# Kernel optimization log

Measured on AMD Instinct MI355X. Metric: run time of the kernel, lower is better.

The kernel has to match this reference:

```python
import jax, jax.numpy as jnp
import numpy as np

C, S, H = 64, 2048, 512
ITERATIONS = 3

def squash(x, eps=1e-07):
    # per-vector squash along last dim: (|x|^2/(1+|x|^2)) * x/|x|
    sq = jnp.sum(x * x, axis=-1, keepdims=True)
    safe_norm = jnp.sqrt(sq + eps)
    scale = sq / (1.0 + sq)
    return scale * (x / safe_norm)

def setup_inputs() -> dict:
    key = jax.random.key(0)
    k1, k2 = jax.random.split(key)
    x = jax.random.normal(k1, (C * S, H), dtype=jnp.float32)
    # xavier-normal init for Linear(H, H)
    std = np.sqrt(2.0 / (H + H)).astype(np.float32)
    W_weight = jax.random.normal(k2, (H, H), dtype=jnp.float32) * std
    W_bias = jnp.zeros((H,), dtype=jnp.float32)
    return {"x": x, "W_weight": W_weight, "W_bias": W_bias}

def reference(x, W_weight, W_bias):
    xr = x.reshape(C, S, H)
    # e_ij = squash(Linear(x))  -> [C, S, H]
    e_ij = squash(jnp.einsum('csh,oh->cso', xr, W_weight) + W_bias)
    b_ij = jnp.zeros((C, S), dtype=x.dtype)
    c_i = jnp.zeros((C, H), dtype=x.dtype)
    for _ in range(ITERATIONS):
        d_i = jax.nn.softmax(b_ij, axis=1)[..., None]          # [C, S, 1]
        c_i = squash(jnp.sum(d_i * e_ij, axis=1))              # [C, H]
        b_ij = b_ij + jnp.einsum('csh,ch->cs', e_ij, c_i)      # [C, S]
    return c_i
```

## Files before the change

kernel.cpp:

```cpp
#include <hip/hip_runtime.h>
#include <hip/hip_bf16.h>
#include <hip/hip_fp16.h>

#define HDIM 512
#define NROWS 131072
#define NCAPS 64

typedef __attribute__((ext_vector_type(8))) short short8;
typedef __attribute__((ext_vector_type(4))) float floatx4;

__device__ __forceinline__ unsigned short f2bf(float f) {
  unsigned u = __float_as_uint(f);
  u += 0x7FFFu + ((u >> 16) & 1u);
  return (unsigned short)(u >> 16);
}
__device__ __forceinline__ float bf2f(unsigned short h) {
  return __uint_as_float(((unsigned)h) << 16);
}

__global__ __launch_bounds__(256) void prep_w_kernel(
    const float* __restrict__ W, unsigned short* __restrict__ wh,
    unsigned short* __restrict__ wl) {
  int i = (blockIdx.x * 256 + threadIdx.x) * 4;
  float4 f = *(const float4*)(W + i);
  float fv[4] = {f.x, f.y, f.z, f.w};
#pragma unroll
  for (int j = 0; j < 4; ++j) {
    unsigned short h = f2bf(fv[j]);
    wh[i + j] = h;
    wl[i + j] = f2bf(fv[j] - bf2f(h));
  }
}

#define BM 128
#define BN 128
#define BK 64

__global__ __launch_bounds__(256) void gemm_kernel(
    const float* __restrict__ x, const unsigned short* __restrict__ wh,
    const unsigned short* __restrict__ wl, const float* __restrict__ bias,
    __half* __restrict__ y, float* __restrict__ sq) {
  __shared__ unsigned short xs[BM * BK];
  __shared__ unsigned short whs[BN * BK];
  __shared__ unsigned short wls[BN * BK];

  const int tid = threadIdx.x;
  const int lane = tid & 63;
  const int widx = tid >> 6;
  const int wave_m = widx >> 1, wave_n = widx & 1;
  const int lrow = lane & 15, quad = lane >> 4, l7 = lane & 7;

  const int bid = blockIdx.x;
  const int m_blk = ((bid >> 5) << 3) + (bid & 7);
  const int n_blk = (bid >> 3) & 3;
  const int row0 = m_blk * BM;
  const int col0 = n_blk * BN;

  floatx4 acc[4][4];
#pragma unroll
  for (int i = 0; i < 4; ++i)
#pragma unroll
    for (int j = 0; j < 4; ++j) acc[i][j] = (floatx4){0.f, 0.f, 0.f, 0.f};

  const int xm = tid >> 3;
  const int xkg = tid & 7;
  const int wn_sub = lane >> 3;
  const int wphys = lane & 7;

  for (int kt = 0; kt < 8; ++kt) {
    const int k0 = kt * BK;
    __syncthreads();
#pragma unroll
    for (int p = 0; p < 4; ++p) {
      int m = p * 32 + xm;
      const float* gp = x + (size_t)(row0 + m) * HDIM + k0 + xkg * 8;
      float4 f0 = *(const float4*)gp;
      float4 f1 = *(const float4*)(gp + 4);
      short8 v;
      v[0] = (short)f2bf(f0.x); v[1] = (short)f2bf(f0.y);
      v[2] = (short)f2bf(f0.z); v[3] = (short)f2bf(f0.w);
      v[4] = (short)f2bf(f1.x); v[5] = (short)f2bf(f1.y);
      v[6] = (short)f2bf(f1.z); v[7] = (short)f2bf(f1.w);
      int phys = xkg ^ (m & 7);
      *(short8*)&xs[m * 64 + phys * 8] = v;
    }
#pragma unroll
    for (int q = 0; q < 4; ++q) {
      int i = widx * 4 + q;
      int n_loc = 8 * i + wn_sub;
      int kg_l = wphys ^ (n_loc & 7);
      size_t goff = (size_t)(col0 + n_loc) * HDIM + k0 + kg_l * 8;
      __builtin_amdgcn_global_load_lds(
          (const __attribute__((address_space(1))) void*)(wh + goff),
          (__attribute__((address_space(3))) void*)&whs[i * 512], 16, 0, 0);
      __builtin_amdgcn_global_load_lds(
          (const __attribute__((address_space(1))) void*)(wl + goff),
          (__attribute__((address_space(3))) void*)&wls[i * 512], 16, 0, 0);
    }
    __syncthreads();
#pragma unroll
    for (int ks = 0; ks < 2; ++ks) {
      int physA = (ks * 4 + quad) ^ l7;
      short8 a[4], bh[4], bl[4];
#pragma unroll
      for (int mt = 0; mt < 4; ++mt) {
        int r = wave_m * 64 + mt * 16 + lrow;
        a[mt] = *(const short8*)&xs[r * 64 + physA * 8];
      }
#pragma unroll
      for (int nt = 0; nt < 4; ++nt) {
        int c = wave_n * 64 + nt * 16 + lrow;
        bh[nt] = *(const short8*)&whs[c * 64 + physA * 8];
        bl[nt] = *(const short8*)&wls[c * 64 + physA * 8];
      }
#pragma unroll
      for (int mt = 0; mt < 4; ++mt)
#pragma unroll
        for (int nt = 0; nt < 4; ++nt) {
          acc[mt][nt] = __builtin_amdgcn_mfma_f32_16x16x32_bf16(
              a[mt], bh[nt], acc[mt][nt], 0, 0, 0);
          acc[mt][nt] = __builtin_amdgcn_mfma_f32_16x16x32_bf16(
              a[mt], bl[nt], acc[mt][nt], 0, 0, 0);
        }
    }
  }

  int colg[4];
  float bias_v[4];
#pragma unroll
  for (int nt = 0; nt < 4; ++nt) {
    colg[nt] = col0 + wave_n * 64 + nt * 16 + lrow;
    bias_v[nt] = bias[colg[nt]];
  }
#pragma unroll
  for (int mt = 0; mt < 4; ++mt) {
#pragma unroll
    for (int r = 0; r < 4; ++r) {
      int rowg = row0 + wave_m * 64 + mt * 16 + quad * 4 + r;
      float s = 0.f;
#pragma unroll
      for (int nt = 0; nt < 4; ++nt) {
        float yv = acc[mt][nt][r] + bias_v[nt];
        s += yv * yv;
        y[(size_t)rowg * HDIM + colg[nt]] = __float2half(yv);
      }
      s += __shfl_xor(s, 1, 64);
      s += __shfl_xor(s, 2, 64);
      s += __shfl_xor(s, 4, 64);
      s += __shfl_xor(s, 8, 64);
      if (lrow == 0) atomicAdd(&sq[rowg], s);
    }
  }
}

__global__ __launch_bounds__(256) void scale_kernel(const float* __restrict__ sq,
                                                    float* __restrict__ scale) {
  int i = blockIdx.x * 256 + threadIdx.x;
  float s = sq[i];
  scale[i] = s / ((1.f + s) * sqrtf(s + 1e-7f));
}

__global__ __launch_bounds__(256) void kbv_kernel(
    const __half* __restrict__ y, const float* __restrict__ scale,
    float* __restrict__ b, const float* __restrict__ c_buf,
    float* __restrict__ u_part, float* __restrict__ den_part) {
  const int wave_g = blockIdx.x * 4 + (threadIdx.x >> 6);
  const int lane = threadIdx.x & 63;
  const int cap = wave_g >> 6;
  const int chunk = wave_g & 63;
  const int r0 = cap * 2048 + chunk * 32;

  float c8[8];
  {
    const float4* cp = (const float4*)(c_buf + cap * HDIM + lane * 8);
    float4 ca = cp[0], cb = cp[1];
    c8[0] = ca.x; c8[1] = ca.y; c8[2] = ca.z; c8[3] = ca.w;
    c8[4] = cb.x; c8[5] = cb.y; c8[6] = cb.z; c8[7] = cb.w;
  }
  float u8[8] = {0, 0, 0, 0, 0, 0, 0, 0};
  float den = 0.f;

  union U { int4 v; __half h[8]; };
  U cur;
  cur.v = *(const int4*)(y + (size_t)r0 * HDIM + lane * 8);

  for (int i = 0; i < 32; ++i) {
    int r = r0 + i;
    U nxt;
    if (i < 31) nxt.v = *(const int4*)(y + (size_t)(r + 1) * HDIM + lane * 8);
    float f[8];
#pragma unroll
    for (int j = 0; j < 8; ++j) f[j] = __half2float(cur.h[j]);
    float dot = f[0] * c8[0] + f[1] * c8[1] + f[2] * c8[2] + f[3] * c8[3] +
                f[4] * c8[4] + f[5] * c8[5] + f[6] * c8[6] + f[7] * c8[7];
    dot += __shfl_xor(dot, 1, 64);
    dot += __shfl_xor(dot, 2, 64);
    dot += __shfl_xor(dot, 4, 64);
    dot += __shfl_xor(dot, 8, 64);
    dot += __shfl_xor(dot, 16, 64);
    dot += __shfl_xor(dot, 32, 64);
    float sc = scale[r];
    float bn = b[r] + sc * dot;
    if (lane == 0) b[r] = bn;
    float w = expf(bn);
    den += w;
    float wsc = w * sc;
#pragma unroll
    for (int j = 0; j < 8; ++j) u8[j] += wsc * f[j];
    cur = nxt;
  }
  float* up = u_part + (size_t)(cap * 64 + chunk) * HDIM + lane * 8;
  *(float4*)up = (float4){u8[0], u8[1], u8[2], u8[3]};
  *(float4*)(up + 4) = (float4){u8[4], u8[5], u8[6], u8[7]};
  if (lane == 0) den_part[cap * 64 + chunk] = den;
}

__global__ __launch_bounds__(256) void kcsq_kernel(
    const float* __restrict__ u_part, const float* __restrict__ den_part,
    float* __restrict__ out) {
  const int cap = blockIdx.x;
  const int t = threadIdx.x;
  __shared__ float red[256];
  __shared__ float sden;

  float d = 0.f;
  if (t < 64) d = den_part[cap * 64 + t];
  red[t] = d;
  __syncthreads();
  if (t == 0) {
    float s = 0.f;
    for (int i = 0; i < 64; ++i) s += red[i];
    sden = s;
  }
  __syncthreads();
  const float den = sden;

  float v0 = 0.f, v1 = 0.f;
  for (int ch = 0; ch < 64; ++ch) {
    const float* up = u_part + (size_t)(cap * 64 + ch) * HDIM;
    v0 += up[t];
    v1 += up[t + 256];
  }
  v0 /= den;
  v1 /= den;

  red[t] = v0 * v0 + v1 * v1;
  __syncthreads();
  for (int s = 128; s > 0; s >>= 1) {
    if (t < s) red[t] += red[t + s];
    __syncthreads();
  }
  const float sqv = red[0];
  const float scv = sqv / ((1.f + sqv) * sqrtf(sqv + 1e-7f));
  out[cap * HDIM + t] = v0 * scv;
  out[cap * HDIM + t + 256] = v1 * scv;
}

extern "C" void kernel_launch(void* const* d_in, const int* in_sizes, int n_in,
                              void* d_out, int out_size, void* d_ws,
                              size_t ws_size, hipStream_t stream) {
  const float* x = (const float*)d_in[0];
  const float* W = (const float*)d_in[1];
  const float* bias = (const float*)d_in[2];
  float* out = (float*)d_out;
  char* ws = (char*)d_ws;

  __half* y = (__half*)ws;
  float* sq = (float*)(ws + (size_t)134217728);
  float* b = sq + 131072;
  float* c_buf = b + 131072;
  float* scale = c_buf + 32768;
  unsigned short* wh = (unsigned short*)(scale + 131072);
  unsigned short* wl = wh + 262144;
  float* u_part = (float*)(wl + 262144);
  float* den_part = u_part + (size_t)64 * 64 * 512;

  hipMemsetAsync(sq, 0, (size_t)(131072 + 131072 + 32768) * sizeof(float),
                 stream);

  prep_w_kernel<<<256, 256, 0, stream>>>(W, wh, wl);
  gemm_kernel<<<4096, 256, 0, stream>>>(x, wh, wl, bias, y, sq);
  scale_kernel<<<512, 256, 0, stream>>>(sq, scale);

  for (int it = 0; it < 3; ++it) {
    kbv_kernel<<<1024, 256, 0, stream>>>(y, scale, b, c_buf, u_part, den_part);
    kcsq_kernel<<<64, 256, 0, stream>>>(u_part, den_part,
                                        (it == 2) ? out : c_buf);
  }
}
```

Before: 586.7 us.

## Switch GEMM to single fp16 MFMA, fuse scale into routing, batch rows

The GEMM now converts x and W to fp16 and runs one f16 MFMA per tile pair, replacing the two-pass bf16 hi/lo split of W. This halves the MFMA work and the weight LDS traffic, at the cost of fp16 range and precision on the inputs (round-toward-zero packing). The separate scale kernel is removed and the squash scale is recomputed inside the routing kernel. That kernel now processes four rows at a time with interleaved shuffles and uses fast exp. The reduce kernel uses 512 threads with one column each.

```diff
diff --git a/kernel.cpp b/kernel.cpp
--- a/kernel.cpp
+++ b/kernel.cpp
@@ -1,35 +1,20 @@
 #include <hip/hip_runtime.h>
-#include <hip/hip_bf16.h>
 #include <hip/hip_fp16.h>
 
 #define HDIM 512
-#define NROWS 131072
-#define NCAPS 64
-
-typedef __attribute__((ext_vector_type(8))) short short8;
+
+typedef __fp16 fp16x2 __attribute__((ext_vector_type(2)));
+typedef _Float16 h8 __attribute__((ext_vector_type(8)));
 typedef __attribute__((ext_vector_type(4))) float floatx4;
 
-__device__ __forceinline__ unsigned short f2bf(float f) {
-  unsigned u = __float_as_uint(f);
-  u += 0x7FFFu + ((u >> 16) & 1u);
-  return (unsigned short)(u >> 16);
-}
-__device__ __forceinline__ float bf2f(unsigned short h) {
-  return __uint_as_float(((unsigned)h) << 16);
-}
-
 __global__ __launch_bounds__(256) void prep_w_kernel(
-    const float* __restrict__ W, unsigned short* __restrict__ wh,
-    unsigned short* __restrict__ wl) {
+    const float* __restrict__ W, _Float16* __restrict__ wf) {
   int i = (blockIdx.x * 256 + threadIdx.x) * 4;
   float4 f = *(const float4*)(W + i);
-  float fv[4] = {f.x, f.y, f.z, f.w};
-#pragma unroll
-  for (int j = 0; j < 4; ++j) {
-    unsigned short h = f2bf(fv[j]);
-    wh[i + j] = h;
-    wl[i + j] = f2bf(fv[j] - bf2f(h));
-  }
+  wf[i + 0] = (_Float16)f.x;
+  wf[i + 1] = (_Float16)f.y;
+  wf[i + 2] = (_Float16)f.z;
+  wf[i + 3] = (_Float16)f.w;
 }
 
 #define BM 128
@@ -37,12 +22,11 @@
 #define BK 64
 
 __global__ __launch_bounds__(256) void gemm_kernel(
-    const float* __restrict__ x, const unsigned short* __restrict__ wh,
-    const unsigned short* __restrict__ wl, const float* __restrict__ bias,
-    __half* __restrict__ y, float* __restrict__ sq) {
-  __shared__ unsigned short xs[BM * BK];
-  __shared__ unsigned short whs[BN * BK];
-  __shared__ unsigned short wls[BN * BK];
+    const float* __restrict__ x, const _Float16* __restrict__ wf,
+    const float* __restrict__ bias, __half* __restrict__ y,
+    float* __restrict__ sq) {
+  __shared__ _Float16 xs[BM * BK];
+  __shared__ _Float16 wsm[BN * BK];
 
   const int tid = threadIdx.x;
   const int lane = tid & 63;
@@ -76,13 +60,13 @@
       const float* gp = x + (size_t)(row0 + m) * HDIM + k0 + xkg * 8;
       float4 f0 = *(const float4*)gp;
       float4 f1 = *(const float4*)(gp + 4);
-      short8 v;
-      v[0] = (short)f2bf(f0.x); v[1] = (short)f2bf(f0.y);
-      v[2] = (short)f2bf(f0.z); v[3] = (short)f2bf(f0.w);
-      v[4] = (short)f2bf(f1.x); v[5] = (short)f2bf(f1.y);
-      v[6] = (short)f2bf(f1.z); v[7] = (short)f2bf(f1.w);
+      union { h8 v8; fp16x2 v2[4]; } u;
+      u.v2[0] = __builtin_amdgcn_cvt_pkrtz(f0.x, f0.y);
+      u.v2[1] = __builtin_amdgcn_cvt_pkrtz(f0.z, f0.w);
+      u.v2[2] = __builtin_amdgcn_cvt_pkrtz(f1.x, f1.y);
+      u.v2[3] = __builtin_amdgcn_cvt_pkrtz(f1.z, f1.w);
       int phys = xkg ^ (m & 7);
-      *(short8*)&xs[m * 64 + phys * 8] = v;
+      *(h8*)&xs[m * 64 + phys * 8] = u.v8;
     }
 #pragma unroll
     for (int q = 0; q < 4; ++q) {
@@ -91,37 +75,30 @@
       int kg_l = wphys ^ (n_loc & 7);
       size_t goff = (size_t)(col0 + n_loc) * HDIM + k0 + kg_l * 8;
       __builtin_amdgcn_global_load_lds(
-          (const __attribute__((address_space(1))) void*)(wh + goff),
-          (__attribute__((address_space(3))) void*)&whs[i * 512], 16, 0, 0);
-      __builtin_amdgcn_global_load_lds(
-          (const __attribute__((address_space(1))) void*)(wl + goff),
-          (__attribute__((address_space(3))) void*)&wls[i * 512], 16, 0, 0);
+          (const __attribute__((address_space(1))) void*)(wf + goff),
+          (__attribute__((address_space(3))) void*)&wsm[i * 512], 16, 0, 0);
     }
     __syncthreads();
 #pragma unroll
     for (int ks = 0; ks < 2; ++ks) {
       int physA = (ks * 4 + quad) ^ l7;
-      short8 a[4], bh[4], bl[4];
+      h8 a[4], bh[4];
 #pragma unroll
       for (int mt = 0; mt < 4; ++mt) {
         int r = wave_m * 64 + mt * 16 + lrow;
-        a[mt] = *(const short8*)&xs[r * 64 + physA * 8];
+        a[mt] = *(const h8*)&xs[r * 64 + physA * 8];
       }
 #pragma unroll
       for (int nt = 0; nt < 4; ++nt) {
         int c = wave_n * 64 + nt * 16 + lrow;
-        bh[nt] = *(const short8*)&whs[c * 64 + physA * 8];
-        bl[nt] = *(const short8*)&wls[c * 64 + physA * 8];
+        bh[nt] = *(const h8*)&wsm[c * 64 + physA * 8];
       }
 #pragma unroll
       for (int mt = 0; mt < 4; ++mt)
 #pragma unroll
-        for (int nt = 0; nt < 4; ++nt) {
-          acc[mt][nt] = __builtin_amdgcn_mfma_f32_16x16x32_bf16(
+        for (int nt = 0; nt < 4; ++nt)
+          acc[mt][nt] = __builtin_amdgcn_mfma_f32_16x16x32_f16(
               a[mt], bh[nt], acc[mt][nt], 0, 0, 0);
-          acc[mt][nt] = __builtin_amdgcn_mfma_f32_16x16x32_bf16(
-              a[mt], bl[nt], acc[mt][nt], 0, 0, 0);
-        }
     }
   }
 
@@ -153,15 +130,8 @@
   }
 }
 
-__global__ __launch_bounds__(256) void scale_kernel(const float* __restrict__ sq,
-                                                    float* __restrict__ scale) {
-  int i = blockIdx.x * 256 + threadIdx.x;
-  float s = sq[i];
-  scale[i] = s / ((1.f + s) * sqrtf(s + 1e-7f));
-}
-
 __global__ __launch_bounds__(256) void kbv_kernel(
-    const __half* __restrict__ y, const float* __restrict__ scale,
+    const __half* __restrict__ y, const float* __restrict__ sqbuf,
     float* __restrict__ b, const float* __restrict__ c_buf,
     float* __restrict__ u_part, float* __restrict__ den_part) {
   const int wave_g = blockIdx.x * 4 + (threadIdx.x >> 6);
@@ -180,34 +150,51 @@
   float u8[8] = {0, 0, 0, 0, 0, 0, 0, 0};
   float den = 0.f;
 
-  union U { int4 v; __half h[8]; };
-  U cur;
-  cur.v = *(const int4*)(y + (size_t)r0 * HDIM + lane * 8);
-
-  for (int i = 0; i < 32; ++i) {
-    int r = r0 + i;
-    U nxt;
-    if (i < 31) nxt.v = *(const int4*)(y + (size_t)(r + 1) * HDIM + lane * 8);
-    float f[8];
-#pragma unroll
-    for (int j = 0; j < 8; ++j) f[j] = __half2float(cur.h[j]);
-    float dot = f[0] * c8[0] + f[1] * c8[1] + f[2] * c8[2] + f[3] * c8[3] +
-                f[4] * c8[4] + f[5] * c8[5] + f[6] * c8[6] + f[7] * c8[7];
-    dot += __shfl_xor(dot, 1, 64);
-    dot += __shfl_xor(dot, 2, 64);
-    dot += __shfl_xor(dot, 4, 64);
-    dot += __shfl_xor(dot, 8, 64);
-    dot += __shfl_xor(dot, 16, 64);
-    dot += __shfl_xor(dot, 32, 64);
-    float sc = scale[r];
-    float bn = b[r] + sc * dot;
-    if (lane == 0) b[r] = bn;
-    float w = expf(bn);
-    den += w;
-    float wsc = w * sc;
-#pragma unroll
-    for (int j = 0; j < 8; ++j) u8[j] += wsc * f[j];
-    cur = nxt;
+  union U { int4 v; __half hh[8]; };
+  U cur[4], nxt[4];
+  const __half* yb = y + (size_t)r0 * HDIM + lane * 8;
+#pragma unroll
+  for (int j = 0; j < 4; ++j) cur[j].v = *(const int4*)(yb + (size_t)j * HDIM);
+
+  for (int g = 0; g < 8; ++g) {
+    const int rg = r0 + g * 4;
+    if (g < 7) {
+#pragma unroll
+      for (int j = 0; j < 4; ++j)
+        nxt[j].v = *(const int4*)(yb + (size_t)(g * 4 + 4 + j) * HDIM);
+    }
+    float sc[4], bv[4];
+#pragma unroll
+    for (int j = 0; j < 4; ++j) {
+      float s = sqbuf[rg + j];
+      sc[j] = s / ((1.f + s) * sqrtf(s + 1e-7f));
+      bv[j] = b[rg + j];
+    }
+    float dot[4];
+#pragma unroll
+    for (int j = 0; j < 4; ++j) {
+      float d = 0.f;
+#pragma unroll
+      for (int k = 0; k < 8; ++k) d += __half2float(cur[j].hh[k]) * c8[k];
+      dot[j] = d;
+    }
+#pragma unroll
+    for (int s = 1; s < 64; s <<= 1) {
+#pragma unroll
+      for (int j = 0; j < 4; ++j) dot[j] += __shfl_xor(dot[j], s, 64);
+    }
+#pragma unroll
+    for (int j = 0; j < 4; ++j) {
+      float bn = bv[j] + sc[j] * dot[j];
+      if (lane == 0) b[rg + j] = bn;
+      float w = __expf(bn);
+      den += w;
+      float wsc = w * sc[j];
+#pragma unroll
+      for (int k = 0; k < 8; ++k) u8[k] += wsc * __half2float(cur[j].hh[k]);
+    }
+#pragma unroll
+    for (int j = 0; j < 4; ++j) cur[j] = nxt[j];
   }
   float* up = u_part + (size_t)(cap * 64 + chunk) * HDIM + lane * 8;
   *(float4*)up = (float4){u8[0], u8[1], u8[2], u8[3]};
@@ -215,45 +202,37 @@
   if (lane == 0) den_part[cap * 64 + chunk] = den;
 }
 
-__global__ __launch_bounds__(256) void kcsq_kernel(
+__global__ __launch_bounds__(512) void kcsq_kernel(
     const float* __restrict__ u_part, const float* __restrict__ den_part,
     float* __restrict__ out) {
   const int cap = blockIdx.x;
   const int t = threadIdx.x;
-  __shared__ float red[256];
-  __shared__ float sden;
-
-  float d = 0.f;
-  if (t < 64) d = den_part[cap * 64 + t];
+  __shared__ float red[512];
+
+  float d = (t < 64) ? den_part[cap * 64 + t] : 0.f;
   red[t] = d;
   __syncthreads();
-  if (t == 0) {
-    float s = 0.f;
-    for (int i = 0; i < 64; ++i) s += red[i];
-    sden = s;
-  }
+  for (int s = 256; s > 0; s >>= 1) {
+    if (t < s) red[t] += red[t + s];
+    __syncthreads();
+  }
+  const float den = red[0];
   __syncthreads();
-  const float den = sden;
-
-  float v0 = 0.f, v1 = 0.f;
-  for (int ch = 0; ch < 64; ++ch) {
-    const float* up = u_part + (size_t)(cap * 64 + ch) * HDIM;
-    v0 += up[t];
-    v1 += up[t + 256];
-  }
-  v0 /= den;
-  v1 /= den;
-
-  red[t] = v0 * v0 + v1 * v1;
+
+  float v = 0.f;
+  const float* up = u_part + (size_t)cap * 64 * HDIM + t;
+  for (int ch = 0; ch < 64; ++ch) v += up[ch * HDIM];
+  v /= den;
+
+  red[t] = v * v;
   __syncthreads();
-  for (int s = 128; s > 0; s >>= 1) {
+  for (int s = 256; s > 0; s >>= 1) {
     if (t < s) red[t] += red[t + s];
     __syncthreads();
   }
   const float sqv = red[0];
   const float scv = sqv / ((1.f + sqv) * sqrtf(sqv + 1e-7f));
-  out[cap * HDIM + t] = v0 * scv;
-  out[cap * HDIM + t + 256] = v1 * scv;
+  out[cap * HDIM + t] = v * scv;
 }
 
 extern "C" void kernel_launch(void* const* d_in, const int* in_sizes, int n_in,
@@ -269,22 +248,20 @@
   float* sq = (float*)(ws + (size_t)134217728);
   float* b = sq + 131072;
   float* c_buf = b + 131072;
-  float* scale = c_buf + 32768;
-  unsigned short* wh = (unsigned short*)(scale + 131072);
-  unsigned short* wl = wh + 262144;
-  float* u_part = (float*)(wl + 262144);
+  _Float16* wf = (_Float16*)(c_buf + 32768);
+  float* u_part = (float*)(wf + 262144);
   float* den_part = u_part + (size_t)64 * 64 * 512;
 
-  hipMemsetAsync(sq, 0, (size_t)(131072 + 131072 + 32768) * sizeof(float),
-                 stream);
-
-  prep_w_kernel<<<256, 256, 0, stream>>>(W, wh, wl);
-  gemm_kernel<<<4096, 256, 0, stream>>>(x, wh, wl, bias, y, sq);
-  scale_kernel<<<512, 256, 0, stream>>>(sq, scale);
+  (void)hipMemsetAsync(sq, 0,
+                       (size_t)(131072 + 131072 + 32768) * sizeof(float),
+                       stream);
+
+  prep_w_kernel<<<256, 256, 0, stream>>>(W, wf);
+  gemm_kernel<<<4096, 256, 0, stream>>>(x, wf, bias, y, sq);
 
   for (int it = 0; it < 3; ++it) {
-    kbv_kernel<<<1024, 256, 0, stream>>>(y, scale, b, c_buf, u_part, den_part);
-    kcsq_kernel<<<64, 256, 0, stream>>>(u_part, den_part,
+    kbv_kernel<<<1024, 256, 0, stream>>>(y, sq, b, c_buf, u_part, den_part);
+    kcsq_kernel<<<64, 512, 0, stream>>>(u_part, den_part,
                                         (it == 2) ? out : c_buf);
   }
 }
```

Measured after the change: 549.6 us. 1.07x faster.
